# Optimization experiments

Hardware: AMD Instinct MI355X
Metric: run time of the kernel (lower is better)

Reference implementation:

```python
import jax, jax.numpy as jnp
import numpy as np

N = 50000   # nodes
E = 600000  # edges
F = 128     # num_features (= in_channels = out_channels of EvolveGCNO)
C = 2       # num_classes


def setup_inputs() -> dict:
    key = jax.random.key(0)
    ks = jax.random.split(key, 8)
    s = 1.0 / np.sqrt(F)
    x = jax.random.normal(ks[0], (N, F), jnp.float32)
    edge_index = jax.random.randint(ks[1], (2, E), 0, N, jnp.int64)
    W0 = jax.random.uniform(ks[2], (F, F), jnp.float32, -s, s)      # initial GCN weight (glorot-ish)
    w_ih = jax.random.uniform(ks[3], (4 * F, F), jnp.float32, -s, s)  # LSTM input-hidden
    w_hh = jax.random.uniform(ks[4], (4 * F, F), jnp.float32, -s, s)  # LSTM hidden-hidden
    b_ih = jax.random.uniform(ks[5], (4 * F,), jnp.float32, -s, s)
    b_hh = jax.random.uniform(ks[6], (4 * F,), jnp.float32, -s, s)
    gcn_bias = jnp.zeros((F,), jnp.float32)
    Wc = jax.random.uniform(ks[7], (C, F), jnp.float32, -s, s)       # classifier nn.Linear(F, C)
    bc = jnp.zeros((C,), jnp.float32)
    return dict(x=x, W0=W0, w_ih=w_ih, w_hh=w_hh, b_ih=b_ih, b_hh=b_hh,
                gcn_bias=gcn_bias, Wc=Wc, bc=bc, edge_index=edge_index)


def reference(x, W0, w_ih, w_hh, b_ih, b_hh, gcn_bias, Wc, bc, edge_index):
    n = x.shape[0]
    # --- EvolveGCN-O weight evolution: one LSTM step on the FxF weight,
    # rows of W0 are the LSTM "batch", initial hidden/cell state are zero.
    gates = W0 @ w_ih.T + b_ih + b_hh            # [F, 4F]  (h=0 so w_hh term vanishes)
    i, f, g, o = jnp.split(gates, 4, axis=1)     # PyTorch gate order: i, f, g, o
    c = jax.nn.sigmoid(i) * jnp.tanh(g)          # c0 = 0 -> f-gate term drops
    W = jax.nn.sigmoid(o) * jnp.tanh(c)          # evolved GCN weight [F, F]

    # --- GCN normalization with self-loops: D^-1/2 (A + I) D^-1/2
    loop = jnp.arange(n, dtype=edge_index.dtype)
    row = jnp.concatenate([edge_index[0], loop])  # source
    col = jnp.concatenate([edge_index[1], loop])  # target
    ew = jnp.ones(row.shape[0], x.dtype)
    deg = jax.ops.segment_sum(ew, col, num_segments=n)
    dis = jnp.where(deg > 0, jax.lax.rsqrt(jnp.maximum(deg, 1.0)), 0.0)
    norm = dis[row] * dis[col]                    # [E+N]

    # --- GCNConv_Fixed_W: transform then aggregate messages at targets
    xw = x @ W                                    # [N, F]
    msg = norm[:, None] * xw[row]                 # gather + scale
    h = jax.ops.segment_sum(msg, col, num_segments=n) + gcn_bias  # scatter-add

    h = jax.nn.relu(h)
    # dropout(p=0.3) is identity in eval mode
    return h @ Wc.T + bc                          # [N, C]
```

## Files before the change

kernel.cpp:

```cpp
#include <hip/hip_runtime.h>
#include <hip/hip_bf16.h>
#include <hip/hip_fp16.h>

#define F 128
#define CAP 32
#define NF 1024
#define OVF_MAX 1024

typedef __bf16 bf16x8 __attribute__((ext_vector_type(8)));
typedef float f32x4 __attribute__((ext_vector_type(4)));

static __device__ __forceinline__ unsigned int f2bfbits(float f) {
  unsigned int u = __float_as_uint(f);
  return (u + 0x7fffu + ((u >> 16) & 1u)) >> 16;
}


__global__ __launch_bounds__(256) void lstm_zero_kernel(
    const float* __restrict__ W0, const float* __restrict__ w_ih,
    const float* __restrict__ b_ih, const float* __restrict__ b_hh,
    unsigned short* __restrict__ Wt, int* __restrict__ deg,
    int* __restrict__ ovf_cnt, int n) {
  __shared__ __align__(16) float srow[4][F];
  __shared__ float sg[4][4 * F];
  int b = blockIdx.x, t = threadIdx.x;
  if (b < 32) {
    int r0 = b * 4;
    for (int i = t; i < 4 * F; i += 256)
      srow[i >> 7][i & 127] = W0[(size_t)(r0 + (i >> 7)) * F + (i & 127)];
    __syncthreads();
#pragma unroll
    for (int half = 0; half < 2; half++) {
      int gc = t + half * 256;
      float acc[4] = {0.f, 0.f, 0.f, 0.f};
      const float4* wv4 = (const float4*)(w_ih + (size_t)gc * F);
#pragma unroll 4
      for (int k4 = 0; k4 < F / 4; k4++) {
        float4 w = wv4[k4];
#pragma unroll
        for (int i = 0; i < 4; i++) {
          float4 s = *(const float4*)&srow[i][k4 * 4];
          acc[i] = fmaf(s.x, w.x, fmaf(s.y, w.y, fmaf(s.z, w.z, fmaf(s.w, w.w, acc[i]))));
        }
      }
      float bias = b_ih[gc] + b_hh[gc];
#pragma unroll
      for (int i = 0; i < 4; i++) sg[i][gc] = acc[i] + bias;
    }
    __syncthreads();
#pragma unroll
    for (int half = 0; half < 2; half++) {
      int idx2 = t + half * 256;
      int rr = idx2 >> 7, c = idx2 & 127;
      float gi = sg[rr][c], gg = sg[rr][c + 2 * F], go = sg[rr][c + 3 * F];
      float si = 1.f / (1.f + expf(-gi));
      float so = 1.f / (1.f + expf(-go));
      float cc2 = si * tanhf(gg);
      Wt[(size_t)c * F + r0 + rr] = (unsigned short)f2bfbits(so * tanhf(cc2));
    }
  } else {
    int stride = ((int)gridDim.x - 32) * 256;
    int4* dz = (int4*)deg;
    int total4 = n * 4;
    const int4 z = make_int4(0, 0, 0, 0);
    for (int i = (b - 32) * 256 + t; i < total4; i += stride) dz[i] = z;
    if (b == 32 && t == 0) *ovf_cnt = 0;
  }
}

__global__ __launch_bounds__(256) void fill_xw_kernel(
    const int* __restrict__ row, const int* __restrict__ col,
    int* __restrict__ deg, unsigned short* __restrict__ bucket,
    int* __restrict__ ovf_cnt, int* __restrict__ ovf,
    const float* __restrict__ x, const unsigned short* __restrict__ Wt,
    unsigned short* __restrict__ xwb, int n, int e) {
  int b = blockIdx.x, t = threadIdx.x;
  if (b < NF) {
    int g = b & 7;
    int cg = b >> 3;
    const int stride = (NF / 8) * 256;
    for (int i = cg * 256 + t; i < e; i += stride) {
      int c = col[i];
      if ((c & 7) == g) {
        int r = row[i];
        int p = atomicAdd(&deg[(size_t)c * 16], 1);
        if (p < CAP) {
          bucket[(size_t)c * CAP + p] = (unsigned short)r;
        } else {
          int q = atomicAdd(ovf_cnt, 1);
          if (q < OVF_MAX) {
            ovf[2 * q + 0] = c;
            ovf[2 * q + 1] = r;
          }
        }
      }
    }
  } else {
    int w = t >> 6, l = t & 63;
    int q = l >> 4, m = l & 15;
    int m0 = (b - NF) * 64 + w * 16;
    int arow = m0 + m;
    bf16x8 a[4];
    const float4* xr4 = (const float4*)(x + (size_t)arow * F);
    bool rv = arow < n;
#pragma unroll
    for (int kc = 0; kc < 4; kc++) {
      uint4 pk = make_uint4(0u, 0u, 0u, 0u);
      if (rv) {
        float4 v0 = xr4[kc * 8 + q * 2 + 0];
        float4 v1 = xr4[kc * 8 + q * 2 + 1];
        pk.x = f2bfbits(v0.x) | (f2bfbits(v0.y) << 16);
        pk.y = f2bfbits(v0.z) | (f2bfbits(v0.w) << 16);
        pk.z = f2bfbits(v1.x) | (f2bfbits(v1.y) << 16);
        pk.w = f2bfbits(v1.z) | (f2bfbits(v1.w) << 16);
      }
      a[kc] = __builtin_bit_cast(bf16x8, pk);
    }
#pragma unroll
    for (int nc = 0; nc < 8; nc++) {
      f32x4 acc = {0.f, 0.f, 0.f, 0.f};
#pragma unroll
      for (int kc = 0; kc < 4; kc++) {
        uint4 bu = *(const uint4*)(Wt + (size_t)(nc * 16 + m) * F + kc * 32 + q * 8);
        acc = __builtin_amdgcn_mfma_f32_16x16x32_bf16(
            a[kc], __builtin_bit_cast(bf16x8, bu), acc, 0, 0, 0);
      }
#pragma unroll
      for (int r = 0; r < 4; r++) {
        int gr = m0 + q * 4 + r;
        if (gr < n)
          xwb[(size_t)gr * F + nc * 16 + m] = (unsigned short)f2bfbits(acc[r]);
      }
    }
  }
}

__global__ __launch_bounds__(256) void scale_kernel(
    const int* __restrict__ deg, unsigned short* __restrict__ xwb, int n) {
  int i = blockIdx.x * 256 + threadIdx.x;
  if (i >= n * 16) return;
  int v = i >> 4;
  float dv = rsqrtf((float)(deg[(size_t)v * 16] + 1));
  uint4 u = ((uint4*)xwb)[i];
  unsigned int w[4] = {u.x, u.y, u.z, u.w};
#pragma unroll
  for (int k = 0; k < 4; k++) {
    float lo = __uint_as_float(w[k] << 16) * dv;
    float hi = __uint_as_float(w[k] & 0xffff0000u) * dv;
    unsigned short hl = __half_as_ushort(__float2half_rn(lo));
    unsigned short hh = __half_as_ushort(__float2half_rn(hi));
    w[k] = (unsigned int)hl | ((unsigned int)hh << 16);
  }
  ((uint4*)xwb)[i] = make_uint4(w[0], w[1], w[2], w[3]);
}

__global__ __launch_bounds__(256) void agg_kernel(
    const int* __restrict__ deg, const unsigned short* __restrict__ bucket,
    const unsigned int* __restrict__ ywb, const int* __restrict__ ovf_cnt,
    const int* __restrict__ ovf, const float* __restrict__ gcn_bias,
    const float* __restrict__ Wc, const float* __restrict__ bc,
    float* __restrict__ out, int n) {
  int wave = threadIdx.x >> 6;
  int lane = threadIdx.x & 63;
  int v = blockIdx.x * 4 + wave;
  if (v >= n) return;
  int d = deg[(size_t)v * 16];
  float dv = rsqrtf((float)(d + 1));
  float ax, ay;
  {
    unsigned int u = ywb[(size_t)v * 64 + lane];
    ax = __half2float(__ushort_as_half((unsigned short)(u & 0xffffu)));
    ay = __half2float(__ushort_as_half((unsigned short)(u >> 16)));
  }
  int eend = d < CAP ? d : CAP;
  const unsigned short* bkt = bucket + (size_t)v * CAP;
  if (eend > 0) {
    uint4 b0 = *(const uint4*)(bkt);
    uint4 b1 = *(const uint4*)(bkt + 8);
    unsigned int wv[8] = {b0.x, b0.y, b0.z, b0.w, b1.x, b1.y, b1.z, b1.w};
    int s[16];
    unsigned int u[16];
#pragma unroll
    for (int q = 0; q < 16; q++) {
      int raw = (q & 1) ? (int)(wv[q >> 1] >> 16) : (int)(wv[q >> 1] & 0xffffu);
      s[q] = (q < eend) ? raw : 0;
    }
#pragma unroll
    for (int q = 0; q < 16; q++) u[q] = ywb[(size_t)s[q] * 64 + lane];
#pragma unroll
    for (int q = 0; q < 16; q++) {
      float msk = (q < eend) ? 1.f : 0.f;
      ax = fmaf(msk, __half2float(__ushort_as_half((unsigned short)(u[q] & 0xffffu))), ax);
      ay = fmaf(msk, __half2float(__ushort_as_half((unsigned short)(u[q] >> 16))), ay);
    }
    for (int j = 16; j < eend; j += 8) {
      int s2[8];
      unsigned int u2[8];
#pragma unroll
      for (int q = 0; q < 8; q++) s2[q] = bkt[j + q < eend ? j + q : 0];
#pragma unroll
      for (int q = 0; q < 8; q++) u2[q] = ywb[(size_t)s2[q] * 64 + lane];
#pragma unroll
      for (int q = 0; q < 8; q++) {
        float msk = (j + q < eend) ? 1.f : 0.f;
        ax = fmaf(msk, __half2float(__ushort_as_half((unsigned short)(u2[q] & 0xffffu))), ax);
        ay = fmaf(msk, __half2float(__ushort_as_half((unsigned short)(u2[q] >> 16))), ay);
      }
    }
  }
  if (d > CAP) {
    int oc = *ovf_cnt;
    if (oc > OVF_MAX) oc = OVF_MAX;
    for (int k = 0; k < oc; k++) {
      if (ovf[2 * k] == v) {
        int s3 = ovf[2 * k + 1];
        unsigned int uu = ywb[(size_t)s3 * 64 + lane];
        ax += __half2float(__ushort_as_half((unsigned short)(uu & 0xffffu)));
        ay += __half2float(__ushort_as_half((unsigned short)(uu >> 16)));
      }
    }
  }
  int f0 = lane * 2;
  float h0 = fmaxf(fmaf(dv, ax, gcn_bias[f0]), 0.f);
  float h1 = fmaxf(fmaf(dv, ay, gcn_bias[f0 + 1]), 0.f);
  float a0 = h0 * Wc[f0] + h1 * Wc[f0 + 1];
  float a1 = h0 * Wc[F + f0] + h1 * Wc[F + f0 + 1];
#pragma unroll
  for (int off = 32; off > 0; off >>= 1) {
    a0 += __shfl_down(a0, off);
    a1 += __shfl_down(a1, off);
  }
  if (lane == 0) {
    out[(size_t)v * 2 + 0] = a0 + bc[0];
    out[(size_t)v * 2 + 1] = a1 + bc[1];
  }
}

extern "C" void kernel_launch(void* const* d_in, const int* in_sizes, int n_in,
                              void* d_out, int out_size, void* d_ws, size_t ws_size,
                              hipStream_t stream) {
  const float* x        = (const float*)d_in[0];
  const float* W0       = (const float*)d_in[1];
  const float* w_ih     = (const float*)d_in[2];
  const float* b_ih     = (const float*)d_in[4];
  const float* b_hh     = (const float*)d_in[5];
  const float* gcn_bias = (const float*)d_in[6];
  const float* Wc       = (const float*)d_in[7];
  const float* bc       = (const float*)d_in[8];
  const int*   ei       = (const int*)d_in[9];

  const int n = in_sizes[0] / F;
  const int e = in_sizes[9] / 2;
  const int* row = ei;
  const int* col = ei + e;

  char* wsb = (char*)d_ws;
  unsigned short* Wt = (unsigned short*)wsb;  wsb += 32768;
  int*   deg     = (int*)wsb;                 wsb += (size_t)n * 64;
  int*   ovf_cnt = (int*)wsb;                 wsb += 256;
  int*   ovf     = (int*)wsb;                 wsb += 8 * OVF_MAX;
  unsigned short* bucket = (unsigned short*)wsb;
  wsb += (size_t)n * CAP * 2;
  unsigned short* xwb = (unsigned short*)wsb;

  const int NT = (n + 63) / 64;

  lstm_zero_kernel<<<32 + 128, 256, 0, stream>>>(W0, w_ih, b_ih, b_hh, Wt,
                                                 deg, ovf_cnt, n);

  fill_xw_kernel<<<NF + NT, 256, 0, stream>>>(row, col, deg, bucket, ovf_cnt,
                                              ovf, x, Wt, xwb, n, e);

  scale_kernel<<<(n * 16 + 255) / 256, 256, 0, stream>>>(deg, xwb, n);

  agg_kernel<<<(n + 3) / 4, 256, 0, stream>>>(deg, bucket,
                                              (const unsigned int*)xwb,
                                              ovf_cnt, ovf, gcn_bias, Wc, bc,
                                              (float*)d_out, n);
}
```

Measured before the change: 157.9 us.

## Replace feature prescale pass with per-node dis array and drop column-group filtering

Removes the pass that rescaled every xw row by its source normalisation and converted it to fp16. A small kernel now writes a compact per-node dis/deg array, and the aggregation applies dis[src] per gathered edge while reading the bf16 features directly. The edge-fill loop also drops its 8-way column-group filter, so each edge is read once instead of by eight block groups. This saves a full read-write pass over the feature matrix and redundant edge reads, but adds a scattered dis load per edge and atomic contention that is no longer grouped by column.

```diff
diff --git a/kernel.cpp b/kernel.cpp
--- a/kernel.cpp
+++ b/kernel.cpp
@@ -1,10 +1,9 @@
 #include <hip/hip_runtime.h>
 #include <hip/hip_bf16.h>
-#include <hip/hip_fp16.h>
 
 #define F 128
 #define CAP 32
-#define NF 1024
+#define NFILL 1024
 #define OVF_MAX 1024
 
 typedef __bf16 bf16x8 __attribute__((ext_vector_type(8)));
@@ -75,30 +74,26 @@
     const float* __restrict__ x, const unsigned short* __restrict__ Wt,
     unsigned short* __restrict__ xwb, int n, int e) {
   int b = blockIdx.x, t = threadIdx.x;
-  if (b < NF) {
-    int g = b & 7;
-    int cg = b >> 3;
-    const int stride = (NF / 8) * 256;
-    for (int i = cg * 256 + t; i < e; i += stride) {
+  if (b < NFILL) {
+    const int stride = NFILL * 256;
+    for (int i = b * 256 + t; i < e; i += stride) {
       int c = col[i];
-      if ((c & 7) == g) {
-        int r = row[i];
-        int p = atomicAdd(&deg[(size_t)c * 16], 1);
-        if (p < CAP) {
-          bucket[(size_t)c * CAP + p] = (unsigned short)r;
-        } else {
-          int q = atomicAdd(ovf_cnt, 1);
-          if (q < OVF_MAX) {
-            ovf[2 * q + 0] = c;
-            ovf[2 * q + 1] = r;
-          }
+      int r = row[i];
+      int p = atomicAdd(&deg[(size_t)c * 16], 1);
+      if (p < CAP) {
+        bucket[(size_t)c * CAP + p] = (unsigned short)r;
+      } else {
+        int q = atomicAdd(ovf_cnt, 1);
+        if (q < OVF_MAX) {
+          ovf[2 * q + 0] = c;
+          ovf[2 * q + 1] = r;
         }
       }
     }
   } else {
     int w = t >> 6, l = t & 63;
     int q = l >> 4, m = l & 15;
-    int m0 = (b - NF) * 64 + w * 16;
+    int m0 = (b - NFILL) * 64 + w * 16;
     int arow = m0 + m;
     bf16x8 a[4];
     const float4* xr4 = (const float4*)(x + (size_t)arow * F);
@@ -135,27 +130,20 @@
   }
 }
 
-__global__ __launch_bounds__(256) void scale_kernel(
-    const int* __restrict__ deg, unsigned short* __restrict__ xwb, int n) {
-  int i = blockIdx.x * 256 + threadIdx.x;
-  if (i >= n * 16) return;
-  int v = i >> 4;
-  float dv = rsqrtf((float)(deg[(size_t)v * 16] + 1));
-  uint4 u = ((uint4*)xwb)[i];
-  unsigned int w[4] = {u.x, u.y, u.z, u.w};
-#pragma unroll
-  for (int k = 0; k < 4; k++) {
-    float lo = __uint_as_float(w[k] << 16) * dv;
-    float hi = __uint_as_float(w[k] & 0xffff0000u) * dv;
-    unsigned short hl = __half_as_ushort(__float2half_rn(lo));
-    unsigned short hh = __half_as_ushort(__float2half_rn(hi));
-    w[k] = (unsigned int)hl | ((unsigned int)hh << 16);
-  }
-  ((uint4*)xwb)[i] = make_uint4(w[0], w[1], w[2], w[3]);
+__global__ __launch_bounds__(256) void dis_kernel(
+    const int* __restrict__ deg, float* __restrict__ dis,
+    int* __restrict__ degc, int n) {
+  int v = blockIdx.x * 256 + threadIdx.x;
+  if (v < n) {
+    int d = deg[(size_t)v * 16];
+    dis[v] = rsqrtf((float)(d + 1));
+    degc[v] = d;
+  }
 }
 
 __global__ __launch_bounds__(256) void agg_kernel(
-    const int* __restrict__ deg, const unsigned short* __restrict__ bucket,
+    const float* __restrict__ dis, const int* __restrict__ degc,
+    const unsigned short* __restrict__ bucket,
     const unsigned int* __restrict__ ywb, const int* __restrict__ ovf_cnt,
     const int* __restrict__ ovf, const float* __restrict__ gcn_bias,
     const float* __restrict__ Wc, const float* __restrict__ bc,
@@ -164,13 +152,13 @@
   int lane = threadIdx.x & 63;
   int v = blockIdx.x * 4 + wave;
   if (v >= n) return;
-  int d = deg[(size_t)v * 16];
-  float dv = rsqrtf((float)(d + 1));
+  int d = degc[v];
+  float dv = dis[v];
   float ax, ay;
   {
     unsigned int u = ywb[(size_t)v * 64 + lane];
-    ax = __half2float(__ushort_as_half((unsigned short)(u & 0xffffu)));
-    ay = __half2float(__ushort_as_half((unsigned short)(u >> 16)));
+    ax = dv * __uint_as_float(u << 16);
+    ay = dv * __uint_as_float(u & 0xffff0000u);
   }
   int eend = d < CAP ? d : CAP;
   const unsigned short* bkt = bucket + (size_t)v * CAP;
@@ -179,6 +167,7 @@
     uint4 b1 = *(const uint4*)(bkt + 8);
     unsigned int wv[8] = {b0.x, b0.y, b0.z, b0.w, b1.x, b1.y, b1.z, b1.w};
     int s[16];
+    float nr[16];
     unsigned int u[16];
 #pragma unroll
     for (int q = 0; q < 16; q++) {
@@ -188,23 +177,28 @@
 #pragma unroll
     for (int q = 0; q < 16; q++) u[q] = ywb[(size_t)s[q] * 64 + lane];
 #pragma unroll
+    for (int q = 0; q < 16; q++)
+      nr[q] = (q < eend) ? dis[s[q]] : 0.f;
+#pragma unroll
     for (int q = 0; q < 16; q++) {
-      float msk = (q < eend) ? 1.f : 0.f;
-      ax = fmaf(msk, __half2float(__ushort_as_half((unsigned short)(u[q] & 0xffffu))), ax);
-      ay = fmaf(msk, __half2float(__ushort_as_half((unsigned short)(u[q] >> 16))), ay);
+      ax = fmaf(nr[q], __uint_as_float(u[q] << 16), ax);
+      ay = fmaf(nr[q], __uint_as_float(u[q] & 0xffff0000u), ay);
     }
     for (int j = 16; j < eend; j += 8) {
       int s2[8];
+      float nr2[8];
       unsigned int u2[8];
 #pragma unroll
       for (int q = 0; q < 8; q++) s2[q] = bkt[j + q < eend ? j + q : 0];
 #pragma unroll
       for (int q = 0; q < 8; q++) u2[q] = ywb[(size_t)s2[q] * 64 + lane];
 #pragma unroll
+      for (int q = 0; q < 8; q++)
+        nr2[q] = (j + q < eend) ? dis[s2[q]] : 0.f;
+#pragma unroll
       for (int q = 0; q < 8; q++) {
-        float msk = (j + q < eend) ? 1.f : 0.f;
-        ax = fmaf(msk, __half2float(__ushort_as_half((unsigned short)(u2[q] & 0xffffu))), ax);
-        ay = fmaf(msk, __half2float(__ushort_as_half((unsigned short)(u2[q] >> 16))), ay);
+        ax = fmaf(nr2[q], __uint_as_float(u2[q] << 16), ax);
+        ay = fmaf(nr2[q], __uint_as_float(u2[q] & 0xffff0000u), ay);
       }
     }
   }
@@ -214,9 +208,10 @@
     for (int k = 0; k < oc; k++) {
       if (ovf[2 * k] == v) {
         int s3 = ovf[2 * k + 1];
+        float nrr = dis[s3];
         unsigned int uu = ywb[(size_t)s3 * 64 + lane];
-        ax += __half2float(__ushort_as_half((unsigned short)(uu & 0xffffu)));
-        ay += __half2float(__ushort_as_half((unsigned short)(uu >> 16)));
+        ax = fmaf(nrr, __uint_as_float(uu << 16), ax);
+        ay = fmaf(nrr, __uint_as_float(uu & 0xffff0000u), ay);
       }
     }
   }
@@ -261,6 +256,8 @@
   int*   ovf     = (int*)wsb;                 wsb += 8 * OVF_MAX;
   unsigned short* bucket = (unsigned short*)wsb;
   wsb += (size_t)n * CAP * 2;
+  float* dis  = (float*)wsb;  wsb += ((size_t)n * 4 + 255) & ~(size_t)255;
+  int*   degc = (int*)wsb;    wsb += ((size_t)n * 4 + 255) & ~(size_t)255;
   unsigned short* xwb = (unsigned short*)wsb;
 
   const int NT = (n + 63) / 64;
@@ -268,12 +265,12 @@
   lstm_zero_kernel<<<32 + 128, 256, 0, stream>>>(W0, w_ih, b_ih, b_hh, Wt,
                                                  deg, ovf_cnt, n);
 
-  fill_xw_kernel<<<NF + NT, 256, 0, stream>>>(row, col, deg, bucket, ovf_cnt,
-                                              ovf, x, Wt, xwb, n, e);
-
-  scale_kernel<<<(n * 16 + 255) / 256, 256, 0, stream>>>(deg, xwb, n);
-
-  agg_kernel<<<(n + 3) / 4, 256, 0, stream>>>(deg, bucket,
+  fill_xw_kernel<<<NFILL + NT, 256, 0, stream>>>(row, col, deg, bucket,
+                                                 ovf_cnt, ovf, x, Wt, xwb, n, e);
+
+  dis_kernel<<<(n + 255) / 256, 256, 0, stream>>>(deg, dis, degc, n);
+
+  agg_kernel<<<(n + 3) / 4, 256, 0, stream>>>(dis, degc, bucket,
                                               (const unsigned int*)xwb,
                                               ovf_cnt, ovf, gcn_bias, Wc, bc,
                                               (float*)d_out, n);
```

New measurement: 178.6 us. 1.13x slower.

## Split bucket fill from XW GEMM and fuse degree scaling into GEMM epilogue

Applied to the files above, without the earlier changes.

The combined fill+GEMM launch becomes two kernels: the edge bucketing kernel runs first, then the X·W MFMA kernel reads the finished degrees and writes D^-1/2-scaled fp16 results directly. This removes the separate scale pass, which re-read and re-wrote the whole bf16 XW buffer, and drops one rounding step. In exchange, the GEMM no longer overlaps with the atomic-heavy fill, so the two phases now run back to back.

```diff
diff --git a/kernel.cpp b/kernel.cpp
--- a/kernel.cpp
+++ b/kernel.cpp
@@ -68,90 +68,79 @@
   }
 }
 
-__global__ __launch_bounds__(256) void fill_xw_kernel(
+__global__ __launch_bounds__(256) void fill_kernel(
     const int* __restrict__ row, const int* __restrict__ col,
     int* __restrict__ deg, unsigned short* __restrict__ bucket,
-    int* __restrict__ ovf_cnt, int* __restrict__ ovf,
+    int* __restrict__ ovf_cnt, int* __restrict__ ovf, int e) {
+  int b = blockIdx.x, t = threadIdx.x;
+  int g = b & 7;
+  int cg = b >> 3;
+  const int stride = (NF / 8) * 256;
+  for (int i = cg * 256 + t; i < e; i += stride) {
+    int c = col[i];
+    if ((c & 7) == g) {
+      int r = row[i];
+      int p = atomicAdd(&deg[(size_t)c * 16], 1);
+      if (p < CAP) {
+        bucket[(size_t)c * CAP + p] = (unsigned short)r;
+      } else {
+        int q = atomicAdd(ovf_cnt, 1);
+        if (q < OVF_MAX) {
+          ovf[2 * q + 0] = c;
+          ovf[2 * q + 1] = r;
+        }
+      }
+    }
+  }
+}
+
+__global__ __launch_bounds__(256) void xw_scale_kernel(
     const float* __restrict__ x, const unsigned short* __restrict__ Wt,
-    unsigned short* __restrict__ xwb, int n, int e) {
+    const int* __restrict__ deg, unsigned short* __restrict__ ywb, int n) {
   int b = blockIdx.x, t = threadIdx.x;
-  if (b < NF) {
-    int g = b & 7;
-    int cg = b >> 3;
-    const int stride = (NF / 8) * 256;
-    for (int i = cg * 256 + t; i < e; i += stride) {
-      int c = col[i];
-      if ((c & 7) == g) {
-        int r = row[i];
-        int p = atomicAdd(&deg[(size_t)c * 16], 1);
-        if (p < CAP) {
-          bucket[(size_t)c * CAP + p] = (unsigned short)r;
-        } else {
-          int q = atomicAdd(ovf_cnt, 1);
-          if (q < OVF_MAX) {
-            ovf[2 * q + 0] = c;
-            ovf[2 * q + 1] = r;
-          }
-        }
-      }
-    }
-  } else {
-    int w = t >> 6, l = t & 63;
-    int q = l >> 4, m = l & 15;
-    int m0 = (b - NF) * 64 + w * 16;
-    int arow = m0 + m;
-    bf16x8 a[4];
-    const float4* xr4 = (const float4*)(x + (size_t)arow * F);
-    bool rv = arow < n;
+  int w = t >> 6, l = t & 63;
+  int q = l >> 4, m = l & 15;
+  int m0 = b * 64 + w * 16;
+  int arow = m0 + m;
+  bf16x8 a[4];
+  const float4* xr4 = (const float4*)(x + (size_t)arow * F);
+  bool rv = arow < n;
+#pragma unroll
+  for (int kc = 0; kc < 4; kc++) {
+    uint4 pk = make_uint4(0u, 0u, 0u, 0u);
+    if (rv) {
+      float4 v0 = xr4[kc * 8 + q * 2 + 0];
+      float4 v1 = xr4[kc * 8 + q * 2 + 1];
+      pk.x = f2bfbits(v0.x) | (f2bfbits(v0.y) << 16);
+      pk.y = f2bfbits(v0.z) | (f2bfbits(v0.w) << 16);
+      pk.z = f2bfbits(v1.x) | (f2bfbits(v1.y) << 16);
+      pk.w = f2bfbits(v1.z) | (f2bfbits(v1.w) << 16);
+    }
+    a[kc] = __builtin_bit_cast(bf16x8, pk);
+  }
+  float disr[4];
+#pragma unroll
+  for (int r = 0; r < 4; r++) {
+    int gr = m0 + q * 4 + r;
+    disr[r] = (gr < n) ? rsqrtf((float)(deg[(size_t)gr * 16] + 1)) : 0.f;
+  }
+#pragma unroll
+  for (int nc = 0; nc < 8; nc++) {
+    f32x4 acc = {0.f, 0.f, 0.f, 0.f};
 #pragma unroll
     for (int kc = 0; kc < 4; kc++) {
-      uint4 pk = make_uint4(0u, 0u, 0u, 0u);
-      if (rv) {
-        float4 v0 = xr4[kc * 8 + q * 2 + 0];
-        float4 v1 = xr4[kc * 8 + q * 2 + 1];
-        pk.x = f2bfbits(v0.x) | (f2bfbits(v0.y) << 16);
-        pk.y = f2bfbits(v0.z) | (f2bfbits(v0.w) << 16);
-        pk.z = f2bfbits(v1.x) | (f2bfbits(v1.y) << 16);
-        pk.w = f2bfbits(v1.z) | (f2bfbits(v1.w) << 16);
-      }
-      a[kc] = __builtin_bit_cast(bf16x8, pk);
-    }
-#pragma unroll
-    for (int nc = 0; nc < 8; nc++) {
-      f32x4 acc = {0.f, 0.f, 0.f, 0.f};
-#pragma unroll
-      for (int kc = 0; kc < 4; kc++) {
-        uint4 bu = *(const uint4*)(Wt + (size_t)(nc * 16 + m) * F + kc * 32 + q * 8);
-        acc = __builtin_amdgcn_mfma_f32_16x16x32_bf16(
-            a[kc], __builtin_bit_cast(bf16x8, bu), acc, 0, 0, 0);
-      }
-#pragma unroll
-      for (int r = 0; r < 4; r++) {
-        int gr = m0 + q * 4 + r;
-        if (gr < n)
-          xwb[(size_t)gr * F + nc * 16 + m] = (unsigned short)f2bfbits(acc[r]);
-      }
-    }
-  }
-}
-
-__global__ __launch_bounds__(256) void scale_kernel(
-    const int* __restrict__ deg, unsigned short* __restrict__ xwb, int n) {
-  int i = blockIdx.x * 256 + threadIdx.x;
-  if (i >= n * 16) return;
-  int v = i >> 4;
-  float dv = rsqrtf((float)(deg[(size_t)v * 16] + 1));
-  uint4 u = ((uint4*)xwb)[i];
-  unsigned int w[4] = {u.x, u.y, u.z, u.w};
-#pragma unroll
-  for (int k = 0; k < 4; k++) {
-    float lo = __uint_as_float(w[k] << 16) * dv;
-    float hi = __uint_as_float(w[k] & 0xffff0000u) * dv;
-    unsigned short hl = __half_as_ushort(__float2half_rn(lo));
-    unsigned short hh = __half_as_ushort(__float2half_rn(hi));
-    w[k] = (unsigned int)hl | ((unsigned int)hh << 16);
-  }
-  ((uint4*)xwb)[i] = make_uint4(w[0], w[1], w[2], w[3]);
+      uint4 bu = *(const uint4*)(Wt + (size_t)(nc * 16 + m) * F + kc * 32 + q * 8);
+      acc = __builtin_amdgcn_mfma_f32_16x16x32_bf16(
+          a[kc], __builtin_bit_cast(bf16x8, bu), acc, 0, 0, 0);
+    }
+#pragma unroll
+    for (int r = 0; r < 4; r++) {
+      int gr = m0 + q * 4 + r;
+      if (gr < n)
+        ywb[(size_t)gr * F + nc * 16 + m] =
+            __half_as_ushort(__float2half_rn(disr[r] * acc[r]));
+    }
+  }
 }
 
 __global__ __launch_bounds__(256) void agg_kernel(
@@ -261,20 +250,19 @@
   int*   ovf     = (int*)wsb;                 wsb += 8 * OVF_MAX;
   unsigned short* bucket = (unsigned short*)wsb;
   wsb += (size_t)n * CAP * 2;
-  unsigned short* xwb = (unsigned short*)wsb;
+  unsigned short* ywb = (unsigned short*)wsb;
 
   const int NT = (n + 63) / 64;
 
   lstm_zero_kernel<<<32 + 128, 256, 0, stream>>>(W0, w_ih, b_ih, b_hh, Wt,
                                                  deg, ovf_cnt, n);
 
-  fill_xw_kernel<<<NF + NT, 256, 0, stream>>>(row, col, deg, bucket, ovf_cnt,
-                                              ovf, x, Wt, xwb, n, e);
-
-  scale_kernel<<<(n * 16 + 255) / 256, 256, 0, stream>>>(deg, xwb, n);
+  fill_kernel<<<NF, 256, 0, stream>>>(row, col, deg, bucket, ovf_cnt, ovf, e);
+
+  xw_scale_kernel<<<NT, 256, 0, stream>>>(x, Wt, deg, ywb, n);
 
   agg_kernel<<<(n + 3) / 4, 256, 0, stream>>>(deg, bucket,
-                                              (const unsigned int*)xwb,
+                                              (const unsigned int*)ywb,
                                               ovf_cnt, ovf, gcn_bias, Wc, bc,
                                               (float*)d_out, n);
 }
```

New measurement: 167.9 us. 1.06x slower.
